# Performance work log

Hardware: AMD Instinct MI355X
Metric: run time of the kernel (lower is better)

Reference implementation:

```python
import jax, jax.numpy as jnp
import numpy as np

B, T, D_IN, H, OUT = 256, 512, 128, 256, 128


def setup_inputs() -> dict:
    key = jax.random.key(0)
    ks = jax.random.split(key, 10)
    s_in = 1.0 / np.sqrt(H)
    inp = {
        "x": jax.random.normal(ks[0], (B, T, D_IN), dtype=jnp.float32),
        # layer 0 (PyTorch LSTM gate order: i, f, g, o along 4H)
        "W_ih0": jax.random.uniform(ks[1], (4 * H, D_IN), minval=-s_in, maxval=s_in),
        "W_hh0": jax.random.uniform(ks[2], (4 * H, H), minval=-s_in, maxval=s_in),
        "b_ih0": jax.random.uniform(ks[3], (4 * H,), minval=-s_in, maxval=s_in),
        "b_hh0": jax.random.uniform(ks[4], (4 * H,), minval=-s_in, maxval=s_in),
        # layer 1
        "W_ih1": jax.random.uniform(ks[5], (4 * H, H), minval=-s_in, maxval=s_in),
        "W_hh1": jax.random.uniform(ks[6], (4 * H, H), minval=-s_in, maxval=s_in),
        "b_ih1": jax.random.uniform(ks[7], (4 * H,), minval=-s_in, maxval=s_in),
        "b_hh1": jax.random.uniform(ks[8], (4 * H,), minval=-s_in, maxval=s_in),
        # fc head (bias=False)
        "W_fc": jax.random.uniform(ks[9], (OUT, H), minval=-s_in, maxval=s_in),
    }
    return inp


def _lstm_layer(x_seq, W_ih, W_hh, b_ih, b_hh):
    # x_seq: [B, T, D]; precompute input projection once (big GEMM),
    # leave only the small h@W_hh GEMM inside the sequential scan.
    b, t = x_seq.shape[0], x_seq.shape[1]
    h_dim = W_hh.shape[1]
    x_proj = jnp.einsum('btd,gd->btg', x_seq, W_ih) + b_ih + b_hh  # [B,T,4H]

    def step(carry, xt):
        h, c = carry
        gates = xt + h @ W_hh.T  # [B,4H]
        i, f, g, o = jnp.split(gates, 4, axis=-1)
        i = jax.nn.sigmoid(i)
        f = jax.nn.sigmoid(f)
        g = jnp.tanh(g)
        o = jax.nn.sigmoid(o)
        c = f * c + i * g
        h = o * jnp.tanh(c)
        return (h, c), h

    init = (jnp.zeros((b, h_dim), x_seq.dtype), jnp.zeros((b, h_dim), x_seq.dtype))
    _, hs = jax.lax.scan(step, init, jnp.swapaxes(x_proj, 0, 1))  # hs: [T,B,H]
    return jnp.swapaxes(hs, 0, 1)  # [B,T,H]


def reference(x, W_ih0, W_hh0, b_ih0, b_hh0, W_ih1, W_hh1, b_ih1, b_hh1, W_fc):
    h0 = _lstm_layer(x, W_ih0, W_hh0, b_ih0, b_hh0)   # [B,T,H]
    h1 = _lstm_layer(h0, W_ih1, W_hh1, b_ih1, b_hh1)  # [B,T,H]
    last = h1[:, -1, :]                               # [B,H]
    return last @ W_fc.T                              # [B,OUT]
```

## Files before the change

kernel.cpp:

```cpp
#include <hip/hip_runtime.h>
#include <stdint.h>

#define T_   512
#define H_   256
#define OUTD 128

typedef unsigned long long u64;
typedef __attribute__((ext_vector_type(8))) short s8v;
typedef __attribute__((ext_vector_type(4))) float f4v;

__device__ __forceinline__ f4v mfma16x16x32(s8v a, s8v b, f4v c) {
  return __builtin_amdgcn_mfma_f32_16x16x32_bf16(a, b, c, 0, 0, 0);
}

__device__ __forceinline__ void split_bf16(float f, short &hi, short &lo) {
  unsigned u  = __float_as_uint(f);
  unsigned uh = u & 0xffff0000u;
  hi = (short)(uh >> 16);
  float r = f - __uint_as_float(uh);
  unsigned ur = __float_as_uint(r);
  lo = (short)((ur + 0x7fffu + ((ur >> 16) & 1u)) >> 16);
}

__device__ __forceinline__ unsigned pack_hilo(float f) {
  short hi, lo; split_bf16(f, hi, lo);
  return ((unsigned)(unsigned short)hi << 16) | (unsigned)(unsigned short)lo;
}

__device__ __forceinline__ float sig_(float x) { return 1.f / (1.f + __expf(-x)); }
__device__ __forceinline__ float th_(float x)  { float e = __expf(2.f * x); return 1.f - 2.f / (e + 1.f); }

struct SMem {
  short xhi[16][264], xlo[16][264];
  short hhi[16][264], hlo[16][264];
  float gl[4][16][17];
  float bias[64];
};

template <int LAYER>
__device__ __forceinline__ void lstm_body(
    SMem* sm,
    const float* __restrict__ xin,
    const float* __restrict__ Wih, const float* __restrict__ Whh,
    const float* __restrict__ bih, const float* __restrict__ bhh,
    u64* bx_x,
    u64* bx_own,
    unsigned* rflag,
    float* h1l,
    int g, int mem)
{
  constexpr int KX  = (LAYER == 0) ? 128 : 256;
  constexpr int NKX = KX / 32;
  constexpr int OD  = (LAYER == 0) ? 4 : 2;
  const int tid = threadIdx.x;
  const int w = tid >> 6, lane = tid & 63, n = lane & 15, q = lane >> 4;
  const int bb = tid >> 4, uu = tid & 15;
  const int B0 = g * 16, U0 = mem * 16;

  s8v wxh[NKX], wxl[NKX], whhh[8], whhl[8];
  {
    const int row = w * 256 + U0 + n;
    #pragma unroll
    for (int kf = 0; kf < NKX; ++kf) {
      s8v vh, vl;
      #pragma unroll
      for (int j = 0; j < 8; ++j) { short hi, lo; split_bf16(Wih[row * KX + kf * 32 + q * 8 + j], hi, lo); vh[j] = hi; vl[j] = lo; }
      wxh[kf] = vh; wxl[kf] = vl;
    }
    #pragma unroll
    for (int kf = 0; kf < 8; ++kf) {
      s8v vh, vl;
      #pragma unroll
      for (int j = 0; j < 8; ++j) { short hi, lo; split_bf16(Whh[row * 256 + kf * 32 + q * 8 + j], hi, lo); vh[j] = hi; vl[j] = lo; }
      whhh[kf] = vh; whhl[kf] = vl;
    }
  }
  if (tid < 64) {
    int gate = tid >> 4, u = tid & 15;
    int grow = gate * 256 + U0 + u;
    sm->bias[tid] = bih[grow] + bhh[grow];
  }

  u64* own = bx_own + (size_t)g * OD * 4096;
  u64* src = (LAYER == 1) ? (bx_x + (size_t)g * 4 * 4096) : nullptr;
  unsigned* rfg    = rflag + g * 256;
  unsigned* rfself = rfg + mem * 16;

  float c = 0.f;

  for (int s = 0; s < T_; ++s) {
    float xv[8];
    if (LAYER == 0) {
      const float* px = xin + ((size_t)(B0 + bb) * T_ + s) * 128 + uu * 8;
      float4 v0 = *(const float4*)px, v1 = *(const float4*)(px + 4);
      xv[0] = v0.x; xv[1] = v0.y; xv[2] = v0.z; xv[3] = v0.w;
      xv[4] = v1.x; xv[5] = v1.y; xv[6] = v1.z; xv[7] = v1.w;
    }

    unsigned rfv = 0xffffffffu;
    if (LAYER == 0 && s >= 4 && w == 0 && lane < 16)
      rfv = __hip_atomic_load(&rfg[lane * 16], __ATOMIC_RELAXED, __HIP_MEMORY_SCOPE_AGENT);

    u64 xp[16];
    if (LAYER == 1) {
      const u64* pbx = src + (size_t)(s & 3) * 4096;
      #pragma unroll
      for (int i = 0; i < 16; ++i)
        xp[i] = __hip_atomic_load(&pbx[i * 256 + tid], __ATOMIC_RELAXED, __HIP_MEMORY_SCOPE_AGENT);
    }

    if (s > 0) {
      const u64* pbh = own + (size_t)((s - 1) & (OD - 1)) * 4096;
      const unsigned htag = (unsigned)s;
      u64 hv64[16]; int it = 0;
      for (;;) {
        bool ok = true;
        #pragma unroll
        for (int i = 0; i < 16; ++i)
          hv64[i] = __hip_atomic_load(&pbh[i * 256 + tid], __ATOMIC_RELAXED, __HIP_MEMORY_SCOPE_AGENT);
        #pragma unroll
        for (int i = 0; i < 16; ++i) ok &= ((unsigned)(hv64[i] >> 32) == htag);
        if (ok) break;
        if (++it >= 50000) break;
        __builtin_amdgcn_s_sleep(1);
      }
      #pragma unroll
      for (int i = 0; i < 16; ++i) {
        unsigned d = (unsigned)hv64[i];
        sm->hhi[i][tid] = (short)(d >> 16);
        sm->hlo[i][tid] = (short)(d & 0xffffu);
      }
    } else {
      #pragma unroll
      for (int i = 0; i < 16; ++i) { sm->hhi[i][tid] = 0; sm->hlo[i][tid] = 0; }
    }

    if (LAYER == 1) {
      const u64* pbx = src + (size_t)(s & 3) * 4096;
      const unsigned xtag = (unsigned)(s + 1);
      bool ok = true;
      #pragma unroll
      for (int i = 0; i < 16; ++i) ok &= ((unsigned)(xp[i] >> 32) == xtag);
      if (!ok) {
        int it = 0;
        for (;;) {
          ok = true;
          #pragma unroll
          for (int i = 0; i < 16; ++i)
            xp[i] = __hip_atomic_load(&pbx[i * 256 + tid], __ATOMIC_RELAXED, __HIP_MEMORY_SCOPE_AGENT);
          #pragma unroll
          for (int i = 0; i < 16; ++i) ok &= ((unsigned)(xp[i] >> 32) == xtag);
          if (ok) break;
          if (++it >= 50000) break;
          __builtin_amdgcn_s_sleep(1);
        }
      }
      #pragma unroll
      for (int i = 0; i < 16; ++i) {
        unsigned d = (unsigned)xp[i];
        sm->xhi[i][tid] = (short)(d >> 16);
        sm->xlo[i][tid] = (short)(d & 0xffffu);
      }
    }

    if (LAYER == 0) {
      s8v vh, vl;
      #pragma unroll
      for (int j = 0; j < 8; ++j) { short hi, lo; split_bf16(xv[j], hi, lo); vh[j] = hi; vl[j] = lo; }
      *(s8v*)&sm->xhi[bb][uu * 8] = vh;
      *(s8v*)&sm->xlo[bb][uu * 8] = vl;
    }
    __syncthreads();

    if (LAYER == 1 && tid == 0)
      __hip_atomic_store(rfself, (unsigned)(s + 1), __ATOMIC_RELAXED, __HIP_MEMORY_SCOPE_AGENT);

    f4v a0 = {0.f, 0.f, 0.f, 0.f}, a1 = a0, a2 = a0;
    #pragma unroll
    for (int kf = 0; kf < NKX; ++kf) {
      s8v ah = *(const s8v*)&sm->xhi[n][kf * 32 + q * 8];
      s8v al = *(const s8v*)&sm->xlo[n][kf * 32 + q * 8];
      a0 = mfma16x16x32(ah, wxh[kf], a0);
      a1 = mfma16x16x32(al, wxh[kf], a1);
      a2 = mfma16x16x32(ah, wxl[kf], a2);
    }
    #pragma unroll
    for (int kf = 0; kf < 8; ++kf) {
      s8v ah = *(const s8v*)&sm->hhi[n][kf * 32 + q * 8];
      s8v al = *(const s8v*)&sm->hlo[n][kf * 32 + q * 8];
      a0 = mfma16x16x32(ah, whhh[kf], a0);
      a1 = mfma16x16x32(al, whhh[kf], a1);
      a2 = mfma16x16x32(ah, whhl[kf], a2);
    }
    f4v D = a0 + (a1 + a2);
    #pragma unroll
    for (int r = 0; r < 4; ++r) sm->gl[w][q * 4 + r][n] = D[r];
    __syncthreads();

    float pi = sm->gl[0][bb][uu] + sm->bias[uu];
    float pf = sm->gl[1][bb][uu] + sm->bias[16 + uu];
    float pg = sm->gl[2][bb][uu] + sm->bias[32 + uu];
    float po = sm->gl[3][bb][uu] + sm->bias[48 + uu];
    float ig = sig_(pi), fg = sig_(pf), gg = th_(pg), og = sig_(po);
    c = fg * c + ig * gg;
    float h = og * th_(c);

    if (LAYER == 0) {
      if (s >= 4 && w == 0) {
        const unsigned tgt = (unsigned)(s - 3);
        bool ok = (lane < 16) ? (rfv >= tgt) : true;
        if (!__all((int)ok)) {
          int it = 0;
          for (;;) {
            unsigned v = (lane < 16)
              ? __hip_atomic_load(&rfg[lane * 16], __ATOMIC_RELAXED, __HIP_MEMORY_SCOPE_AGENT)
              : tgt;
            if (__all((int)(v >= tgt))) break;
            if (++it >= 50000) break;
            __builtin_amdgcn_s_sleep(1);
          }
        }
      }
      __syncthreads();
    }

    u64 val = ((u64)(unsigned)(s + 1) << 32) | (u64)pack_hilo(h);
    __hip_atomic_store(&own[(size_t)(s & (OD - 1)) * 4096 + bb * 256 + U0 + uu], val,
                       __ATOMIC_RELAXED, __HIP_MEMORY_SCOPE_AGENT);

    if (LAYER == 1 && s == T_ - 1)
      h1l[(B0 + bb) * H_ + U0 + uu] = h;
  }
}

__global__ __launch_bounds__(256, 2) void lstm_fused(
    const float* __restrict__ x,
    const float* __restrict__ Wih0, const float* __restrict__ Whh0,
    const float* __restrict__ bih0, const float* __restrict__ bhh0,
    const float* __restrict__ Wih1, const float* __restrict__ Whh1,
    const float* __restrict__ bih1, const float* __restrict__ bhh1,
    u64* bx0, u64* bx1, unsigned* rflag, float* h1l)
{
  __shared__ SMem sm;
  const int bid = blockIdx.x;
  if (bid < 256) {
    lstm_body<0>(&sm, x, Wih0, Whh0, bih0, bhh0, nullptr, bx0, rflag, nullptr,
                 bid >> 4, bid & 15);
  } else {
    const int b = bid - 256;
    lstm_body<1>(&sm, nullptr, Wih1, Whh1, bih1, bhh1, bx0, bx1, rflag, h1l,
                 b >> 4, b & 15);
  }
}

__global__ void fc_kernel(const float* __restrict__ h1l, const float* __restrict__ Wfc,
                          float* __restrict__ out) {
  __shared__ float hs[H_];
  const int b = blockIdx.x, o = threadIdx.x;
  hs[o]       = h1l[b * H_ + o];
  hs[o + 128] = h1l[b * H_ + o + 128];
  __syncthreads();
  float acc = 0.f;
  #pragma unroll 8
  for (int u = 0; u < H_; u += 4) {
    float4 wv = *(const float4*)&Wfc[o * H_ + u];
    acc += wv.x * hs[u] + wv.y * hs[u + 1] + wv.z * hs[u + 2] + wv.w * hs[u + 3];
  }
  out[b * OUTD + o] = acc;
}

extern "C" void kernel_launch(void* const* d_in, const int* in_sizes, int n_in,
                              void* d_out, int out_size, void* d_ws, size_t ws_size,
                              hipStream_t stream) {
  const float* x    = (const float*)d_in[0];
  const float* Wih0 = (const float*)d_in[1];
  const float* Whh0 = (const float*)d_in[2];
  const float* bih0 = (const float*)d_in[3];
  const float* bhh0 = (const float*)d_in[4];
  const float* Wih1 = (const float*)d_in[5];
  const float* Whh1 = (const float*)d_in[6];
  const float* bih1 = (const float*)d_in[7];
  const float* bhh1 = (const float*)d_in[8];
  const float* Wfc  = (const float*)d_in[9];

  u64*      bx0   = (u64*)d_ws;
  u64*      bx1   = bx0 + 262144;
  unsigned* rflag = (unsigned*)(bx1 + 131072);
  float*    h1l   = (float*)(rflag + 4096);

  hipMemsetAsync(rflag, 0, 4096 * sizeof(unsigned), stream);

  lstm_fused<<<512, 256, 0, stream>>>(x, Wih0, Whh0, bih0, bhh0,
                                      Wih1, Whh1, bih1, bhh1,
                                      bx0, bx1, rflag, h1l);
  fc_kernel<<<256, 128, 0, stream>>>(h1l, Wfc, (float*)d_out);
}
```

Baseline: 2.785 ms.

## Give each LSTM block 32 hidden units to halve block count

```diff
diff --git a/kernel.cpp b/kernel.cpp
--- a/kernel.cpp
+++ b/kernel.cpp
@@ -33,8 +33,8 @@
 struct SMem {
   short xhi[16][264], xlo[16][264];
   short hhi[16][264], hlo[16][264];
-  float gl[4][16][17];
-  float bias[64];
+  float gl[4][16][33];
+  float bias[128];
 };
 
 template <int LAYER>
@@ -55,38 +55,39 @@
   const int tid = threadIdx.x;
   const int w = tid >> 6, lane = tid & 63, n = lane & 15, q = lane >> 4;
   const int bb = tid >> 4, uu = tid & 15;
-  const int B0 = g * 16, U0 = mem * 16;
-
-  s8v wxh[NKX], wxl[NKX], whhh[8], whhl[8];
-  {
-    const int row = w * 256 + U0 + n;
+  const int B0 = g * 16, U0 = mem * 32;
+
+  s8v wxh[2][NKX], wxl[2][NKX], whhh[2][8], whhl[2][8];
+  #pragma unroll
+  for (int t = 0; t < 2; ++t) {
+    const int row = w * 256 + U0 + t * 16 + n;
     #pragma unroll
     for (int kf = 0; kf < NKX; ++kf) {
       s8v vh, vl;
       #pragma unroll
       for (int j = 0; j < 8; ++j) { short hi, lo; split_bf16(Wih[row * KX + kf * 32 + q * 8 + j], hi, lo); vh[j] = hi; vl[j] = lo; }
-      wxh[kf] = vh; wxl[kf] = vl;
+      wxh[t][kf] = vh; wxl[t][kf] = vl;
     }
     #pragma unroll
     for (int kf = 0; kf < 8; ++kf) {
       s8v vh, vl;
       #pragma unroll
       for (int j = 0; j < 8; ++j) { short hi, lo; split_bf16(Whh[row * 256 + kf * 32 + q * 8 + j], hi, lo); vh[j] = hi; vl[j] = lo; }
-      whhh[kf] = vh; whhl[kf] = vl;
-    }
-  }
-  if (tid < 64) {
-    int gate = tid >> 4, u = tid & 15;
+      whhh[t][kf] = vh; whhl[t][kf] = vl;
+    }
+  }
+  if (tid < 128) {
+    int gate = tid >> 5, u = tid & 31;
     int grow = gate * 256 + U0 + u;
     sm->bias[tid] = bih[grow] + bhh[grow];
   }
 
   u64* own = bx_own + (size_t)g * OD * 4096;
   u64* src = (LAYER == 1) ? (bx_x + (size_t)g * 4 * 4096) : nullptr;
-  unsigned* rfg    = rflag + g * 256;
+  unsigned* rfg    = rflag + g * 128;
   unsigned* rfself = rfg + mem * 16;
 
-  float c = 0.f;
+  float c0 = 0.f, c1 = 0.f;
 
   for (int s = 0; s < T_; ++s) {
     float xv[8];
@@ -98,7 +99,7 @@
     }
 
     unsigned rfv = 0xffffffffu;
-    if (LAYER == 0 && s >= 4 && w == 0 && lane < 16)
+    if (LAYER == 0 && s >= 4 && w == 0 && lane < 8)
       rfv = __hip_atomic_load(&rfg[lane * 16], __ATOMIC_RELAXED, __HIP_MEMORY_SCOPE_AGENT);
 
     u64 xp[16];
@@ -175,44 +176,68 @@
     if (LAYER == 1 && tid == 0)
       __hip_atomic_store(rfself, (unsigned)(s + 1), __ATOMIC_RELAXED, __HIP_MEMORY_SCOPE_AGENT);
 
-    f4v a0 = {0.f, 0.f, 0.f, 0.f}, a1 = a0, a2 = a0;
+    f4v a00 = {0.f,0.f,0.f,0.f}, a01 = a00, a02 = a00;
+    f4v a10 = a00, a11 = a00, a12 = a00;
     #pragma unroll
     for (int kf = 0; kf < NKX; ++kf) {
       s8v ah = *(const s8v*)&sm->xhi[n][kf * 32 + q * 8];
       s8v al = *(const s8v*)&sm->xlo[n][kf * 32 + q * 8];
-      a0 = mfma16x16x32(ah, wxh[kf], a0);
-      a1 = mfma16x16x32(al, wxh[kf], a1);
-      a2 = mfma16x16x32(ah, wxl[kf], a2);
+      a00 = mfma16x16x32(ah, wxh[0][kf], a00);
+      a01 = mfma16x16x32(al, wxh[0][kf], a01);
+      a02 = mfma16x16x32(ah, wxl[0][kf], a02);
+      a10 = mfma16x16x32(ah, wxh[1][kf], a10);
+      a11 = mfma16x16x32(al, wxh[1][kf], a11);
+      a12 = mfma16x16x32(ah, wxl[1][kf], a12);
     }
     #pragma unroll
     for (int kf = 0; kf < 8; ++kf) {
       s8v ah = *(const s8v*)&sm->hhi[n][kf * 32 + q * 8];
       s8v al = *(const s8v*)&sm->hlo[n][kf * 32 + q * 8];
-      a0 = mfma16x16x32(ah, whhh[kf], a0);
-      a1 = mfma16x16x32(al, whhh[kf], a1);
-      a2 = mfma16x16x32(ah, whhl[kf], a2);
-    }
-    f4v D = a0 + (a1 + a2);
-    #pragma unroll
-    for (int r = 0; r < 4; ++r) sm->gl[w][q * 4 + r][n] = D[r];
+      a00 = mfma16x16x32(ah, whhh[0][kf], a00);
+      a01 = mfma16x16x32(al, whhh[0][kf], a01);
+      a02 = mfma16x16x32(ah, whhl[0][kf], a02);
+      a10 = mfma16x16x32(ah, whhh[1][kf], a10);
+      a11 = mfma16x16x32(al, whhh[1][kf], a11);
+      a12 = mfma16x16x32(ah, whhl[1][kf], a12);
+    }
+    f4v D0 = a00 + (a01 + a02);
+    f4v D1 = a10 + (a11 + a12);
+    #pragma unroll
+    for (int r = 0; r < 4; ++r) {
+      sm->gl[w][q * 4 + r][n]      = D0[r];
+      sm->gl[w][q * 4 + r][16 + n] = D1[r];
+    }
     __syncthreads();
 
-    float pi = sm->gl[0][bb][uu] + sm->bias[uu];
-    float pf = sm->gl[1][bb][uu] + sm->bias[16 + uu];
-    float pg = sm->gl[2][bb][uu] + sm->bias[32 + uu];
-    float po = sm->gl[3][bb][uu] + sm->bias[48 + uu];
-    float ig = sig_(pi), fg = sig_(pf), gg = th_(pg), og = sig_(po);
-    c = fg * c + ig * gg;
-    float h = og * th_(c);
+    float h0v, h1v;
+    {
+      float pi = sm->gl[0][bb][uu] + sm->bias[uu];
+      float pf = sm->gl[1][bb][uu] + sm->bias[32 + uu];
+      float pg = sm->gl[2][bb][uu] + sm->bias[64 + uu];
+      float po = sm->gl[3][bb][uu] + sm->bias[96 + uu];
+      float ig = sig_(pi), fg = sig_(pf), gg = th_(pg), og = sig_(po);
+      c0 = fg * c0 + ig * gg;
+      h0v = og * th_(c0);
+    }
+    {
+      int u = uu + 16;
+      float pi = sm->gl[0][bb][u] + sm->bias[u];
+      float pf = sm->gl[1][bb][u] + sm->bias[32 + u];
+      float pg = sm->gl[2][bb][u] + sm->bias[64 + u];
+      float po = sm->gl[3][bb][u] + sm->bias[96 + u];
+      float ig = sig_(pi), fg = sig_(pf), gg = th_(pg), og = sig_(po);
+      c1 = fg * c1 + ig * gg;
+      h1v = og * th_(c1);
+    }
 
     if (LAYER == 0) {
       if (s >= 4 && w == 0) {
         const unsigned tgt = (unsigned)(s - 3);
-        bool ok = (lane < 16) ? (rfv >= tgt) : true;
+        bool ok = (lane < 8) ? (rfv >= tgt) : true;
         if (!__all((int)ok)) {
           int it = 0;
           for (;;) {
-            unsigned v = (lane < 16)
+            unsigned v = (lane < 8)
               ? __hip_atomic_load(&rfg[lane * 16], __ATOMIC_RELAXED, __HIP_MEMORY_SCOPE_AGENT)
               : tgt;
             if (__all((int)(v >= tgt))) break;
@@ -224,16 +249,19 @@
       __syncthreads();
     }
 
-    u64 val = ((u64)(unsigned)(s + 1) << 32) | (u64)pack_hilo(h);
-    __hip_atomic_store(&own[(size_t)(s & (OD - 1)) * 4096 + bb * 256 + U0 + uu], val,
-                       __ATOMIC_RELAXED, __HIP_MEMORY_SCOPE_AGENT);
-
-    if (LAYER == 1 && s == T_ - 1)
-      h1l[(B0 + bb) * H_ + U0 + uu] = h;
-  }
-}
-
-__global__ __launch_bounds__(256, 2) void lstm_fused(
+    const u64 tagw = (u64)(unsigned)(s + 1) << 32;
+    u64* slot = own + (size_t)(s & (OD - 1)) * 4096 + bb * 256 + U0 + uu;
+    __hip_atomic_store(slot,      tagw | (u64)pack_hilo(h0v), __ATOMIC_RELAXED, __HIP_MEMORY_SCOPE_AGENT);
+    __hip_atomic_store(slot + 16, tagw | (u64)pack_hilo(h1v), __ATOMIC_RELAXED, __HIP_MEMORY_SCOPE_AGENT);
+
+    if (LAYER == 1 && s == T_ - 1) {
+      h1l[(B0 + bb) * H_ + U0 + uu]      = h0v;
+      h1l[(B0 + bb) * H_ + U0 + 16 + uu] = h1v;
+    }
+  }
+}
+
+__global__ __launch_bounds__(256, 1) void lstm_fused(
     const float* __restrict__ x,
     const float* __restrict__ Wih0, const float* __restrict__ Whh0,
     const float* __restrict__ bih0, const float* __restrict__ bhh0,
@@ -243,13 +271,13 @@
 {
   __shared__ SMem sm;
   const int bid = blockIdx.x;
-  if (bid < 256) {
+  if (bid < 128) {
     lstm_body<0>(&sm, x, Wih0, Whh0, bih0, bhh0, nullptr, bx0, rflag, nullptr,
-                 bid >> 4, bid & 15);
+                 bid >> 3, bid & 7);
   } else {
-    const int b = bid - 256;
+    const int b = bid - 128;
     lstm_body<1>(&sm, nullptr, Wih1, Whh1, bih1, bhh1, bx0, bx1, rflag, h1l,
-                 b >> 4, b & 15);
+                 b >> 3, b & 7);
   }
 }
 
@@ -290,7 +318,7 @@
 
   hipMemsetAsync(rflag, 0, 4096 * sizeof(unsigned), stream);
 
-  lstm_fused<<<512, 256, 0, stream>>>(x, Wih0, Whh0, bih0, bhh0,
+  lstm_fused<<<256, 256, 0, stream>>>(x, Wih0, Whh0, bih0, bhh0,
                                       Wih1, Whh1, bih1, bhh1,
                                       bx0, bx1, rflag, h1l);
   fc_kernel<<<256, 128, 0, stream>>>(h1l, Wfc, (float*)d_out);
```

Measured after the change: 2.456 ms. 1.13x faster.
